# Performance work log

Measured on AMD Instinct MI355X. Metric: run time of the kernel, lower is better.

Reference implementation:

```python
import jax, jax.numpy as jnp
import numpy as np

HIDDEN = 2048
N_HEADS = 32
N_KV_HEADS = 8
HEAD_DIM = 64
ROPE_THETA = 500000.0
B, S = 1, 2048


def _rope_tables(seq_len):
    inv_freq = 1.0 / ROPE_THETA ** (jnp.arange(0, HEAD_DIM, 2, dtype=jnp.float32) / HEAD_DIM)
    angles = jnp.arange(seq_len, dtype=jnp.float32)[:, None] * inv_freq[None, :]
    return jnp.cos(angles), jnp.sin(angles)


def _apply_rope(x, cos, sin):
    # x: (B, S, H, D); cos/sin: (S, D//2)
    x1 = x[..., 0::2]
    x2 = x[..., 1::2]
    c = cos[None, :, None, :]
    s = sin[None, :, None, :]
    x1r = x1 * c - x2 * s
    x2r = x1 * s + x2 * c
    return jnp.stack([x1r, x2r], axis=-1).reshape(x.shape)


def setup_inputs() -> dict:
    key = jax.random.key(0)
    ks = jax.random.split(key, 5)
    hidden_states = jax.random.normal(ks[0], (B, S, HIDDEN), dtype=jnp.float32)
    # causal mask, broadcastable over (B, H, S, S)
    attention_mask = jnp.tril(jnp.ones((S, S), dtype=bool))[None, :, :]
    sc = 1.0 / np.sqrt(HIDDEN)
    wq = jax.random.normal(ks[1], (HIDDEN, N_HEADS * HEAD_DIM), dtype=jnp.float32) * sc
    wk = jax.random.normal(ks[2], (HIDDEN, N_KV_HEADS * HEAD_DIM), dtype=jnp.float32) * sc
    wv = jax.random.normal(ks[3], (HIDDEN, N_KV_HEADS * HEAD_DIM), dtype=jnp.float32) * sc
    wo = jax.random.normal(ks[4], (N_HEADS * HEAD_DIM, HIDDEN), dtype=jnp.float32) * sc
    return {"hidden_states": hidden_states, "attention_mask": attention_mask,
            "wq": wq, "wk": wk, "wv": wv, "wo": wo}


def reference(hidden_states, attention_mask, wq, wk, wv, wo):
    b, s, _ = hidden_states.shape
    groups = N_HEADS // N_KV_HEADS
    q = (hidden_states @ wq).reshape(b, s, N_HEADS, HEAD_DIM)
    k = (hidden_states @ wk).reshape(b, s, N_KV_HEADS, HEAD_DIM)
    v = (hidden_states @ wv).reshape(b, s, N_KV_HEADS, HEAD_DIM)
    cos, sin = _rope_tables(s)
    q = _apply_rope(q, cos, sin)
    k = _apply_rope(k, cos, sin)
    k = jnp.repeat(k, groups, axis=2)  # (b, s, H, D)
    v = jnp.repeat(v, groups, axis=2)
    q = q.transpose(0, 2, 1, 3)  # (b, H, s, D)
    k = k.transpose(0, 2, 1, 3)
    v = v.transpose(0, 2, 1, 3)
    scores = jnp.einsum('bhqd,bhkd->bhqk', q, k) / jnp.sqrt(jnp.float32(HEAD_DIM))
    scores = jnp.where(attention_mask[:, None, :, :], scores, -jnp.inf)
    probs = jax.nn.softmax(scores, axis=-1)
    out = jnp.einsum('bhqk,bhkd->bhqd', probs, v)
    out = out.transpose(0, 2, 1, 3).reshape(b, s, N_HEADS * HEAD_DIM)
    return out @ wo
```

## Files before the change

### kernel.cpp

```cpp
#include <hip/hip_runtime.h>

typedef __attribute__((ext_vector_type(8))) short short8;
typedef __attribute__((ext_vector_type(4))) float float4v;

union U4S8 { uint4 u; short8 s; };

__device__ __forceinline__ float bf2f(ushort u) {
    union { uint i; float f; } v; v.i = ((uint)u) << 16; return v.f;
}
__device__ __forceinline__ ushort f2bf(float f) {
    union { uint i; float f; } v; v.f = f;
    return (ushort)((v.i + 0x7FFFu + ((v.i >> 16) & 1u)) >> 16);
}
#if __has_builtin(__builtin_amdgcn_cvt_pk_bf16_f32)
__device__ __forceinline__ uint f2bf_pk(float a, float b) {
    auto r = __builtin_amdgcn_cvt_pk_bf16_f32(a, b);
    return __builtin_bit_cast(uint, r);
}
#else
__device__ __forceinline__ uint f2bf_pk(float a, float b) {
    return (uint)f2bf(a) | ((uint)f2bf(b) << 16);
}
#endif
__device__ __forceinline__ void gld_lds16(const ushort* g, ushort* l) {
    __builtin_amdgcn_global_load_lds((const __attribute__((address_space(1))) unsigned int*)g,
                                     (__attribute__((address_space(3))) unsigned int*)l,
                                     16, 0, 0);
}

__device__ __forceinline__ void tconv_body(const float* in, ushort* out,
                                           int C, int r0, int c0, int tid) {
    __shared__ float t[64][65];
    const int lrow = tid >> 2;
    const int lc   = (tid & 3) * 16;
    const float* ip = in + (size_t)(r0 + lrow) * C + c0 + lc;
#pragma unroll
    for (int i = 0; i < 4; i++) {
        float4 v = *(const float4*)(ip + 4 * i);
        t[lrow][lc + 4 * i + 0] = v.x; t[lrow][lc + 4 * i + 1] = v.y;
        t[lrow][lc + 4 * i + 2] = v.z; t[lrow][lc + 4 * i + 3] = v.w;
    }
    __syncthreads();
    ushort* op = out + (size_t)(c0 + lrow) * 2048 + r0 + lc;
#pragma unroll
    for (int i = 0; i < 8; i++)
        ((uint*)op)[i] = f2bf_pk(t[lc + 2 * i][lrow], t[lc + 2 * i + 1][lrow]);
}

__global__ __launch_bounds__(256) void prep(const float* __restrict__ hidden,
                                            const float* __restrict__ wq,
                                            const float* __restrict__ wk,
                                            const float* __restrict__ wv,
                                            ushort* __restrict__ hid,
                                            ushort* __restrict__ wT) {
    const int bx = blockIdx.x;
    if (bx < 2048) {
        const size_t i = ((size_t)bx * 256 + threadIdx.x) * 8;
        float4 a = *(const float4*)(hidden + i);
        float4 b = *(const float4*)(hidden + i + 4);
        uint4 u;
        u.x = f2bf_pk(a.x, a.y); u.y = f2bf_pk(a.z, a.w);
        u.z = f2bf_pk(b.x, b.y); u.w = f2bf_pk(b.z, b.w);
        *(uint4*)(hid + i) = u;
    } else {
        const int i = bx - 2048;
        const int xx = i % 48, yy = i / 48;
        const float* in; ushort* op; int C, cx;
        if (xx < 32)      { in = wq; op = wT;                        C = 2048; cx = xx; }
        else if (xx < 40) { in = wk; op = wT + (size_t)2048 * 2048;  C = 512;  cx = xx - 32; }
        else              { in = wv; op = wT + (size_t)2560 * 2048;  C = 512;  cx = xx - 40; }
        tconv_body(in, op, C, yy * 64, cx * 64, threadIdx.x);
    }
}

__global__ __launch_bounds__(256) void tconv(const float* __restrict__ in,
                                             ushort* __restrict__ out) {
    tconv_body(in, out, 2048, blockIdx.y * 64, blockIdx.x * 64, threadIdx.x);
}

template <bool BF16OUT>
__global__ __launch_bounds__(256) void gemm_n64(const ushort* __restrict__ A,
                                                const ushort* __restrict__ Bt,
                                                void* __restrict__ Cout,
                                                int N, int K, int lda) {
    __shared__ ushort As[128 * 32];
    __shared__ ushort Bs[64 * 32];

    const int tid = threadIdx.x, w = tid >> 6, lane = tid & 63;
    const int lr = lane & 15, quad = lane >> 4;
    const int m0 = blockIdx.x * 128, n0 = blockIdx.y * 64;

    const int srow = lane >> 2;
    const int skb  = (lane & 3) ^ ((srow >> 1) & 3);

    float4v acc[2][4];
#pragma unroll
    for (int a = 0; a < 2; a++)
#pragma unroll
        for (int b = 0; b < 4; b++) { acc[a][b][0] = 0.f; acc[a][b][1] = 0.f; acc[a][b][2] = 0.f; acc[a][b][3] = 0.f; }

    const int fsw = (lr >> 1) & 3;

    for (int k0 = 0; k0 < K; k0 += 32) {
        __syncthreads();
#pragma unroll
        for (int i = 0; i < 2; i++) {
            const int rt = 2 * w + i;
            gld_lds16(A + (size_t)(m0 + rt * 16 + srow) * lda + k0 + skb * 8, &As[rt * 512]);
        }
        gld_lds16(Bt + (size_t)(n0 + w * 16 + srow) * K + k0 + skb * 8, &Bs[w * 512]);
        __syncthreads();

        short8 af[2], bf[4];
#pragma unroll
        for (int mt = 0; mt < 2; mt++)
            af[mt] = *(const short8*)&As[(w * 32 + mt * 16 + lr) * 32 + (quad ^ fsw) * 8];
#pragma unroll
        for (int nt = 0; nt < 4; nt++)
            bf[nt] = *(const short8*)&Bs[(nt * 16 + lr) * 32 + (quad ^ fsw) * 8];
#pragma unroll
        for (int mt = 0; mt < 2; mt++)
#pragma unroll
            for (int nt = 0; nt < 4; nt++)
                acc[mt][nt] = __builtin_amdgcn_mfma_f32_16x16x32_bf16(af[mt], bf[nt], acc[mt][nt], 0, 0, 0);
    }

    const int rbase = m0 + w * 32 + quad * 4;
    const int cbase = n0 + lr;
#pragma unroll
    for (int mt = 0; mt < 2; mt++)
#pragma unroll
        for (int nt = 0; nt < 4; nt++)
#pragma unroll
            for (int r = 0; r < 4; r++) {
                const size_t idx = (size_t)(rbase + mt * 16 + r) * N + cbase + nt * 16;
                if (BF16OUT) ((ushort*)Cout)[idx] = f2bf(acc[mt][nt][r]);
                else         ((float*)Cout)[idx]  = acc[mt][nt][r];
            }
}

__global__ __launch_bounds__(256) void rope_bf(ushort* __restrict__ Qb,
                                               ushort* __restrict__ Kc) {
    const int idx = blockIdx.x * 256 + threadIdx.x;
    const int QP = 2048 * 1024;
    int s, p; ushort* base; float osc;
    if (idx < QP) { s = idx >> 10; p = idx & 1023; base = Qb; osc = 0.18033688f; }
    else { int r = idx - QP; s = r >> 8; p = r & 255; base = Kc; osc = 1.0f; }
    const int j = p & 31;
    float inv = __expf(-(float)(2 * j) * (1.0f / 64.0f) * 13.122363377404328f);
    float sn, c;
    sincosf((float)s * inv, &sn, &c);
    uint* p2 = (uint*)(base + (size_t)s * 3072 + 2 * p);
    uint xv = *p2;
    float x1 = bf2f((ushort)(xv & 0xFFFFu)), x2 = bf2f((ushort)(xv >> 16));
    *p2 = f2bf_pk((x1 * c - x2 * sn) * osc, (x1 * sn + x2 * c) * osc);
}

__global__ __launch_bounds__(256) void attn_mfma(const ushort* __restrict__ Q,
                                                 const ushort* __restrict__ Kc,
                                                 const ushort* __restrict__ Vc,
                                                 ushort* __restrict__ O0,
                                                 ushort* __restrict__ O1,
                                                 float* __restrict__ L0,
                                                 float* __restrict__ L1) {
    __shared__ ushort Ks[2][64 * 64];
    __shared__ ushort Vt[2][64 * 64];
    __shared__ ushort Ps[4][16 * 64];

    const int tid = threadIdx.x, w = tid >> 6, lane = tid & 63;
    const int lr = lane & 15, quad = lane >> 4;
    const int h = blockIdx.y, g = h >> 2, z = blockIdx.z;

    const int dg = tid & 15;
    const int kl = tid >> 4;
    const int ksub = lane >> 3, dsub = lane & 7;
    ushort* Pw = Ps[w];
    ushort* Op = z ? O1 : O0;
    float*  Lp = z ? L1 : L0;

    const ushort* Vp0 = Vc + g * 64 + dg * 4 + (size_t)3072 * kl;
    const ushort* Kp0 = Kc + g * 64 + ((dsub ^ ksub) * 8) + (size_t)3072 * ksub;

    short8 onesf;
#pragma unroll
    for (int j = 0; j < 8; j++) onesf[j] = (short)0x3F80;

    for (int ti = 0; ti < 2; ti++) {
        const int bx = ti ? 31 - (int)blockIdx.x : (int)blockIdx.x;
        const int nch = (bx >= z) ? ((bx - z) >> 1) + 1 : 0;
        const int last = z + 2 * (nch - 1);

        const ushort* qp = Q + (size_t)(bx * 64 + w * 16 + lr) * 3072 + h * 64 + quad * 8;
        const short8 qf0 = *(const short8*)qp;
        const short8 qf1 = *(const short8*)(qp + 32);

        float4v oacc[4], lacc;
#pragma unroll
        for (int t = 0; t < 4; t++) { oacc[t][0] = 0.f; oacc[t][1] = 0.f; oacc[t][2] = 0.f; oacc[t][3] = 0.f; }
        lacc[0] = 0.f; lacc[1] = 0.f; lacc[2] = 0.f; lacc[3] = 0.f;

        uint2 vv[4];
        if (nch) {
#pragma unroll
            for (int t = 0; t < 4; t++)
                vv[t] = *(const uint2*)(Vp0 + (size_t)(z * 64 + 16 * t) * 3072);
        }
        __syncthreads();
        if (nch) {
#pragma unroll
            for (int i = 0; i < 2; i++) {
                const int rt = 2 * w + i;
                gld_lds16(Kp0 + (size_t)(z * 64 + rt * 8) * 3072, &Ks[0][rt * 512]);
            }
        }

        for (int c = 0; c < nch; c++) {
            const int kb = z + 2 * c;
            const int b = c & 1;
            ushort* bKs = Ks[b];
            ushort* bVt = Vt[b];

#pragma unroll
            for (int i = 0; i < 4; i++) {
                const uint sel = (i & 1) ? 0x07060302u : 0x05040100u;
                uint s0 = (i < 2) ? vv[0].x : vv[0].y;
                uint s1 = (i < 2) ? vv[1].x : vv[1].y;
                uint s2 = (i < 2) ? vv[2].x : vv[2].y;
                uint s3 = (i < 2) ? vv[3].x : vv[3].y;
                uint2 pk;
                pk.x = __builtin_amdgcn_perm(s1, s0, sel);
                pk.y = __builtin_amdgcn_perm(s3, s2, sel);
                *(uint2*)&bVt[(dg * 4 + i) * 64 + (kl ^ ((dg & 3) * 4 + i)) * 4] = pk;
            }

            const int kn = (c + 1 < nch) ? kb + 2 : last;
#pragma unroll
            for (int t = 0; t < 4; t++)
                vv[t] = *(const uint2*)(Vp0 + (size_t)(kn * 64 + 16 * t) * 3072);

            asm volatile("s_waitcnt vmcnt(4) lgkmcnt(0)\n\ts_barrier" ::: "memory");

#pragma unroll
            for (int i = 0; i < 2; i++) {
                const int rt = 2 * w + i;
                gld_lds16(Kp0 + (size_t)(kn * 64 + rt * 8) * 3072, &Ks[1 - b][rt * 512]);
            }

            float4v sacc[4];
#pragma unroll
            for (int t = 0; t < 4; t++) { sacc[t][0] = 0.f; sacc[t][1] = 0.f; sacc[t][2] = 0.f; sacc[t][3] = 0.f; }
#pragma unroll
            for (int t = 0; t < 4; t++) {
                const int krow = t * 16 + lr;
                const int sw = lr & 7;
                short8 kf0 = *(const short8*)&bKs[krow * 64 + ((quad)     ^ sw) * 8];
                short8 kf1 = *(const short8*)&bKs[krow * 64 + ((quad + 4) ^ sw) * 8];
                sacc[t] = __builtin_amdgcn_mfma_f32_16x16x32_bf16(qf0, kf0, sacc[t], 0, 0, 0);
                sacc[t] = __builtin_amdgcn_mfma_f32_16x16x32_bf16(qf1, kf1, sacc[t], 0, 0, 0);
            }

            if (kb == bx) {
#pragma unroll
                for (int r = 0; r < 4; r++) {
                    const int qr = w * 16 + quad * 4 + r;
                    float p0 = exp2f(sacc[0][r]), p1 = exp2f(sacc[1][r]);
                    float p2 = exp2f(sacc[2][r]), p3 = exp2f(sacc[3][r]);
                    if (lr > qr)      p0 = 0.f;
                    if (16 + lr > qr) p1 = 0.f;
                    if (32 + lr > qr) p2 = 0.f;
                    if (48 + lr > qr) p3 = 0.f;
                    const int prow = quad * 4 + r;
                    uint2 pk; pk.x = f2bf_pk(p0, p1); pk.y = f2bf_pk(p2, p3);
                    *(uint2*)&Pw[prow * 64 + (lr ^ prow) * 4] = pk;
                }
            } else {
#pragma unroll
                for (int r = 0; r < 4; r++) {
                    const int prow = quad * 4 + r;
                    uint2 pk;
                    pk.x = f2bf_pk(exp2f(sacc[0][r]), exp2f(sacc[1][r]));
                    pk.y = f2bf_pk(exp2f(sacc[2][r]), exp2f(sacc[3][r]));
                    *(uint2*)&Pw[prow * 64 + (lr ^ prow) * 4] = pk;
                }
            }

#pragma unroll
            for (int ks2 = 0; ks2 < 2; ks2++) {
                const int ub = ks2 * 8 + quad * 2;
                U4S8 pu;
                uint2 plo = *(const uint2*)&Pw[lr * 64 + ((ub)     ^ lr) * 4];
                uint2 phi = *(const uint2*)&Pw[lr * 64 + ((ub + 1) ^ lr) * 4];
                pu.u.x = plo.x; pu.u.y = plo.y; pu.u.z = phi.x; pu.u.w = phi.y;
                lacc = __builtin_amdgcn_mfma_f32_16x16x32_bf16(pu.s, onesf, lacc, 0, 0, 0);
#pragma unroll
                for (int t = 0; t < 4; t++) {
                    const int d = t * 16 + lr;
                    U4S8 vu;
                    uint2 vlo = *(const uint2*)&bVt[d * 64 + ((ub)     ^ lr) * 4];
                    uint2 vhi = *(const uint2*)&bVt[d * 64 + ((ub + 1) ^ lr) * 4];
                    vu.u.x = vlo.x; vu.u.y = vlo.y; vu.u.z = vhi.x; vu.u.w = vhi.y;
                    oacc[t] = __builtin_amdgcn_mfma_f32_16x16x32_bf16(pu.s, vu.s, oacc[t], 0, 0, 0);
                }
            }
        }

        ushort* op = Op + (size_t)(bx * 64 + w * 16 + quad * 4) * 2048 + h * 64 + lr;
#pragma unroll
        for (int t = 0; t < 4; t++)
#pragma unroll
            for (int r = 0; r < 4; r++)
                op[(size_t)r * 2048 + t * 16] = f2bf(oacc[t][r]);
        if (lr == 0) {
#pragma unroll
            for (int r = 0; r < 4; r++)
                Lp[h * 2048 + bx * 64 + w * 16 + quad * 4 + r] = lacc[r];
        }
    }
}

__global__ __launch_bounds__(256) void combine(const ushort* __restrict__ O0,
                                               const ushort* __restrict__ O1,
                                               const float* __restrict__ L0,
                                               const float* __restrict__ L1,
                                               ushort* __restrict__ Ab) {
    const int idx = blockIdx.x * 256 + threadIdx.x;
    const int r = idx >> 8;
    const int c8 = (idx & 255) * 8;
    const int h = c8 >> 6;
    const float rl = 1.0f / (L0[h * 2048 + r] + L1[h * 2048 + r]);
    uint4 a = *(const uint4*)(O0 + (size_t)r * 2048 + c8);
    uint4 b = *(const uint4*)(O1 + (size_t)r * 2048 + c8);
    uint ua[4] = {a.x, a.y, a.z, a.w}, ub[4] = {b.x, b.y, b.z, b.w};
    uint4 res;
    uint rr[4];
#pragma unroll
    for (int k = 0; k < 4; k++) {
        float x0 = bf2f((ushort)(ua[k] & 0xFFFFu)) + bf2f((ushort)(ub[k] & 0xFFFFu));
        float x1 = bf2f((ushort)(ua[k] >> 16))     + bf2f((ushort)(ub[k] >> 16));
        rr[k] = f2bf_pk(x0 * rl, x1 * rl);
    }
    res.x = rr[0]; res.y = rr[1]; res.z = rr[2]; res.w = rr[3];
    *(uint4*)(Ab + (size_t)r * 3072 + c8) = res;
}

extern "C" void kernel_launch(void* const* d_in, const int* in_sizes, int n_in,
                              void* d_out, int out_size, void* d_ws, size_t ws_size,
                              hipStream_t stream) {
    const float* hidden = (const float*)d_in[0];
    const float* wq = (const float*)d_in[2];
    const float* wk = (const float*)d_in[3];
    const float* wv = (const float*)d_in[4];
    const float* wo = (const float*)d_in[5];

    ushort* ws = (ushort*)d_ws;
    ushort* hid  = ws;
    ushort* wT   = ws + 4194304;
    ushort* QKV  = ws + 10485760;
    ushort* Qb = QKV;
    ushort* Kc = QKV + 2048;
    ushort* Vc = QKV + 2560;
    ushort* O1 = (ushort*)d_out;
    float*  L0 = (float*)((ushort*)d_out + 4194304);
    float*  L1 = L0 + 65536;

    prep<<<3584, 256, 0, stream>>>(hidden, wq, wk, wv, hid, wT);
    gemm_n64<true><<<dim3(16, 48), 256, 0, stream>>>(hid, wT, QKV, 3072, 2048, 2048);
    tconv<<<dim3(32, 32), 256, 0, stream>>>(wo, wT);
    rope_bf<<<10240, 256, 0, stream>>>(Qb, Kc);
    attn_mfma<<<dim3(16, 32, 2), 256, 0, stream>>>(Qb, Kc, Vc, hid , O1, L0, L1);
    combine<<<2048, 256, 0, stream>>>(hid, O1, L0, L1, Qb );
    gemm_n64<false><<<dim3(16, 32), 256, 0, stream>>>(Qb, wT, d_out, 2048, 2048, 3072);
}
```

Baseline: 251.9 us.

## Double-buffer GEMM LDS tiles and fuse rope with wo transpose kernel

The GEMM main loop now uses two LDS buffers and issues the next K-slice's global-to-LDS loads before computing on the current slice. This replaces two barriers per iteration with one explicit waitcnt plus barrier, so global latency can overlap MFMA work. Separately, the rope kernel and the wo transpose-convert kernel are merged into one launch to save a launch and let the two independent jobs run side by side. Double buffering doubles LDS use per block, which could lower occupancy, and the explicit waitcnt still waits on all loads at the top of each iteration.

```diff
diff --git a/kernel.cpp b/kernel.cpp
--- a/kernel.cpp
+++ b/kernel.cpp
@@ -73,9 +73,29 @@
     }
 }
 
-__global__ __launch_bounds__(256) void tconv(const float* __restrict__ in,
-                                             ushort* __restrict__ out) {
-    tconv_body(in, out, 2048, blockIdx.y * 64, blockIdx.x * 64, threadIdx.x);
+__global__ __launch_bounds__(256) void mid(ushort* __restrict__ Qb,
+                                           ushort* __restrict__ Kc,
+                                           const float* __restrict__ wo,
+                                           ushort* __restrict__ woT) {
+    const int bx = blockIdx.x;
+    if (bx < 10240) {
+        const int idx = bx * 256 + threadIdx.x;
+        const int QP = 2048 * 1024;
+        int s, p; ushort* base; float osc;
+        if (idx < QP) { s = idx >> 10; p = idx & 1023; base = Qb; osc = 0.18033688f; }
+        else { int r = idx - QP; s = r >> 8; p = r & 255; base = Kc; osc = 1.0f; }
+        const int j = p & 31;
+        float inv = __expf(-(float)(2 * j) * (1.0f / 64.0f) * 13.122363377404328f);
+        float sn, c;
+        sincosf((float)s * inv, &sn, &c);
+        uint* p2 = (uint*)(base + (size_t)s * 3072 + 2 * p);
+        uint xv = *p2;
+        float x1 = bf2f((ushort)(xv & 0xFFFFu)), x2 = bf2f((ushort)(xv >> 16));
+        *p2 = f2bf_pk((x1 * c - x2 * sn) * osc, (x1 * sn + x2 * c) * osc);
+    } else {
+        const int i = bx - 10240;
+        tconv_body(wo, woT, 2048, (i >> 5) * 64, (i & 31) * 64, threadIdx.x);
+    }
 }
 
 template <bool BF16OUT>
@@ -83,8 +103,8 @@
                                                 const ushort* __restrict__ Bt,
                                                 void* __restrict__ Cout,
                                                 int N, int K, int lda) {
-    __shared__ ushort As[128 * 32];
-    __shared__ ushort Bs[64 * 32];
+    __shared__ ushort As[2][128 * 32];
+    __shared__ ushort Bs[2][64 * 32];
 
     const int tid = threadIdx.x, w = tid >> 6, lane = tid & 63;
     const int lr = lane & 15, quad = lane >> 4;
@@ -93,6 +113,9 @@
     const int srow = lane >> 2;
     const int skb  = (lane & 3) ^ ((srow >> 1) & 3);
 
+    const ushort* Ap = A  + (size_t)(m0 + srow) * lda + skb * 8;
+    const ushort* Bp = Bt + (size_t)(n0 + w * 16 + srow) * K + skb * 8;
+
     float4v acc[2][4];
 #pragma unroll
     for (int a = 0; a < 2; a++)
@@ -101,23 +124,36 @@
 
     const int fsw = (lr >> 1) & 3;
 
-    for (int k0 = 0; k0 < K; k0 += 32) {
-        __syncthreads();
-#pragma unroll
-        for (int i = 0; i < 2; i++) {
-            const int rt = 2 * w + i;
-            gld_lds16(A + (size_t)(m0 + rt * 16 + srow) * lda + k0 + skb * 8, &As[rt * 512]);
-        }
-        gld_lds16(Bt + (size_t)(n0 + w * 16 + srow) * K + k0 + skb * 8, &Bs[w * 512]);
-        __syncthreads();
+#pragma unroll
+    for (int i = 0; i < 2; i++) {
+        const int rt = 2 * w + i;
+        gld_lds16(Ap + (size_t)(rt * 16) * lda, &As[0][rt * 512]);
+    }
+    gld_lds16(Bp, &Bs[0][w * 512]);
+
+    const int niter = K >> 5;
+    for (int it = 0; it < niter; it++) {
+        const int b = it & 1;
+
+        asm volatile("s_waitcnt vmcnt(0) lgkmcnt(0)\n\ts_barrier" ::: "memory");
+
+        if (it + 1 < niter) {
+            const int k1 = (it + 1) << 5;
+#pragma unroll
+            for (int i = 0; i < 2; i++) {
+                const int rt = 2 * w + i;
+                gld_lds16(Ap + (size_t)(rt * 16) * lda + k1, &As[1 - b][rt * 512]);
+            }
+            gld_lds16(Bp + k1, &Bs[1 - b][w * 512]);
+        }
 
         short8 af[2], bf[4];
 #pragma unroll
         for (int mt = 0; mt < 2; mt++)
-            af[mt] = *(const short8*)&As[(w * 32 + mt * 16 + lr) * 32 + (quad ^ fsw) * 8];
+            af[mt] = *(const short8*)&As[b][(w * 32 + mt * 16 + lr) * 32 + (quad ^ fsw) * 8];
 #pragma unroll
         for (int nt = 0; nt < 4; nt++)
-            bf[nt] = *(const short8*)&Bs[(nt * 16 + lr) * 32 + (quad ^ fsw) * 8];
+            bf[nt] = *(const short8*)&Bs[b][(nt * 16 + lr) * 32 + (quad ^ fsw) * 8];
 #pragma unroll
         for (int mt = 0; mt < 2; mt++)
 #pragma unroll
@@ -137,23 +173,6 @@
                 if (BF16OUT) ((ushort*)Cout)[idx] = f2bf(acc[mt][nt][r]);
                 else         ((float*)Cout)[idx]  = acc[mt][nt][r];
             }
-}
-
-__global__ __launch_bounds__(256) void rope_bf(ushort* __restrict__ Qb,
-                                               ushort* __restrict__ Kc) {
-    const int idx = blockIdx.x * 256 + threadIdx.x;
-    const int QP = 2048 * 1024;
-    int s, p; ushort* base; float osc;
-    if (idx < QP) { s = idx >> 10; p = idx & 1023; base = Qb; osc = 0.18033688f; }
-    else { int r = idx - QP; s = r >> 8; p = r & 255; base = Kc; osc = 1.0f; }
-    const int j = p & 31;
-    float inv = __expf(-(float)(2 * j) * (1.0f / 64.0f) * 13.122363377404328f);
-    float sn, c;
-    sincosf((float)s * inv, &sn, &c);
-    uint* p2 = (uint*)(base + (size_t)s * 3072 + 2 * p);
-    uint xv = *p2;
-    float x1 = bf2f((ushort)(xv & 0xFFFFu)), x2 = bf2f((ushort)(xv >> 16));
-    *p2 = f2bf_pk((x1 * c - x2 * sn) * osc, (x1 * sn + x2 * c) * osc);
 }
 
 __global__ __launch_bounds__(256) void attn_mfma(const ushort* __restrict__ Q,
@@ -365,8 +384,7 @@
 
     prep<<<3584, 256, 0, stream>>>(hidden, wq, wk, wv, hid, wT);
     gemm_n64<true><<<dim3(16, 48), 256, 0, stream>>>(hid, wT, QKV, 3072, 2048, 2048);
-    tconv<<<dim3(32, 32), 256, 0, stream>>>(wo, wT);
-    rope_bf<<<10240, 256, 0, stream>>>(Qb, Kc);
+    mid<<<11264, 256, 0, stream>>>(Qb, Kc, wo, wT);
     attn_mfma<<<dim3(16, 32, 2), 256, 0, stream>>>(Qb, Kc, Vc, hid , O1, L0, L1);
     combine<<<2048, 256, 0, stream>>>(hid, O1, L0, L1, Qb );
     gemm_n64<false><<<dim3(16, 32), 256, 0, stream>>>(Qb, wT, d_out, 2048, 2048, 3072);
```

New measurement: 243.3 us. 1.04x faster.
